# Kernel tuning notes

Hardware: AMD Instinct MI355X
Metric: run time of the kernel (lower is better)

## Reference

```python
import jax, jax.numpy as jnp
import numpy as np

D_MODEL = 512
N_HEADS = 8
HEAD_SIZE = 64


def setup_inputs() -> dict:
    key = jax.random.key(0)
    ks = jax.random.split(key, 6)
    B, T = 4, 2048
    x_q = jax.random.normal(ks[0], (B, T, D_MODEL), dtype=jnp.float32)
    s = 1.0 / np.sqrt(D_MODEL)
    # per-head q/k/v projection weights, stacked: [H, head_size, d_model]
    Wq = jax.random.normal(ks[1], (N_HEADS, HEAD_SIZE, D_MODEL), dtype=jnp.float32) * s
    Wk = jax.random.normal(ks[2], (N_HEADS, HEAD_SIZE, D_MODEL), dtype=jnp.float32) * s
    Wv = jax.random.normal(ks[3], (N_HEADS, HEAD_SIZE, D_MODEL), dtype=jnp.float32) * s
    Wp = jax.random.normal(ks[4], (D_MODEL, D_MODEL), dtype=jnp.float32) * s
    bp = jax.random.normal(ks[5], (D_MODEL,), dtype=jnp.float32) * 0.01
    return {"x_q": x_q, "Wq": Wq, "Wk": Wk, "Wv": Wv, "Wp": Wp, "bp": bp}


def reference(x_q, Wq, Wk, Wv, Wp, bp):
    B, T, C = x_q.shape  # C == d_model
    # per-head projections: [B, H, T, K]
    q = jnp.einsum('btd,hkd->bhtk', x_q, Wq)
    k = jnp.einsum('btd,hkd->bhtk', x_q, Wk)
    v = jnp.einsum('btd,hkd->bhtk', x_q, Wv)
    # NOTE: original scales by C**-0.5 with C = d_model (not head_size)
    scores = jnp.einsum('bhtk,bhsk->bhts', q, k) * (C ** -0.5)
    causal = jnp.tril(jnp.ones((T, T), dtype=bool))
    scores = jnp.where(causal, scores, -jnp.inf)
    wei = jax.nn.softmax(scores, axis=-1)  # dropout is identity in eval
    out = jnp.einsum('bhts,bhsk->bhtk', wei, v)
    # concat heads: [B, T, H*K] == [B, T, d_model]
    out = out.transpose(0, 2, 1, 3).reshape(B, T, C)
    return out @ Wp.T + bp
```

## Files before the change

kernel.cpp:

```cpp
#include <hip/hip_runtime.h>
#include <hip/hip_bf16.h>

using bf16x8 = __attribute__((ext_vector_type(8))) __bf16;
using f32x4  = __attribute__((ext_vector_type(4))) float;
using f32x16 = __attribute__((ext_vector_type(16))) float;
using i32x4  = __attribute__((ext_vector_type(4))) int;

#define MFMA_16x16x32(a, b, c) __builtin_amdgcn_mfma_f32_16x16x32_bf16((a), (b), (c), 0, 0, 0)
#define MFMA32(a, b, c)        __builtin_amdgcn_mfma_f32_32x32x16_bf16((a), (b), (c), 0, 0, 0)

__device__ __forceinline__ ushort f2bf(float f) {
    return __builtin_bit_cast(ushort, (__bf16)f);
}
__device__ __forceinline__ unsigned pk_bf16(float lo, float hi) {
    unsigned r;
    asm volatile("v_cvt_pk_bf16_f32 %0, %1, %2" : "=v"(r) : "v"(lo), "v"(hi));
    return r;
}
__device__ __forceinline__ void pl32_swap(unsigned &a, unsigned &b) {
    asm volatile("v_permlane32_swap_b32 %0, %1" : "+v"(a), "+v"(b));
}

__global__ __launch_bounds__(256) void cvt_bf16(
    const float* __restrict__ in, ushort* __restrict__ out, int n)
{
    const int i = (blockIdx.x * 256 + threadIdx.x) * 8;
    if (i + 8 <= n) {
        const f32x4 a = *(const f32x4*)(in + i);
        const f32x4 b = *(const f32x4*)(in + i + 4);
        union { ushort u[8]; i32x4 w; } p;
        #pragma unroll
        for (int j = 0; j < 4; ++j) { p.u[j] = f2bf(a[j]); p.u[4 + j] = f2bf(b[j]); }
        *(i32x4*)(out + i) = p.w;
    }
}

__global__ __launch_bounds__(256) void gemm_qkv3(
    const ushort* __restrict__ A, const float* __restrict__ Wq,
    const float* __restrict__ Wk, const float* __restrict__ Wv,
    float qscale, ushort* __restrict__ qb, ushort* __restrict__ kb,
    ushort* __restrict__ vb)
{
    __shared__ ushort lA[128][40];
    __shared__ ushort lB[128][40];
    const int wsel = blockIdx.y >> 2;
    const int n0 = (blockIdx.y & 3) * 128;
    const float* W = (wsel == 0) ? Wq : ((wsel == 1) ? Wk : Wv);
    ushort* out = (wsel == 0) ? qb : ((wsel == 1) ? kb : vb);
    const float scale = (wsel == 0) ? qscale : 1.0f;

    const int m0 = blockIdx.x * 128;
    const int tid  = threadIdx.x;
    const int lane = tid & 63;
    const int wave = tid >> 6;
    const int wr = (wave >> 1) * 64, wc = (wave & 1) * 64;
    const int frow = lane & 15, fk = (lane >> 4) * 8;
    const int sr = tid >> 1, scc = (tid & 1) * 16;

    f32x4 acc[4][4] = {};

    for (int k0 = 0; k0 < 512; k0 += 32) {
        const ushort* pa = A + (m0 + sr) * 512 + k0 + scc;
        const i32x4 va0 = *(const i32x4*)(pa);
        const i32x4 va1 = *(const i32x4*)(pa + 8);
        const float* pb = W + (n0 + sr) * 512 + k0 + scc;
        const f32x4 b0 = *(const f32x4*)(pb);
        const f32x4 b1 = *(const f32x4*)(pb + 4);
        const f32x4 b2 = *(const f32x4*)(pb + 8);
        const f32x4 b3 = *(const f32x4*)(pb + 12);
        union { ushort u[16]; i32x4 w[2]; } pB;
        #pragma unroll
        for (int j = 0; j < 4; ++j) {
            pB.u[j]      = f2bf(b0[j]);  pB.u[4 + j]  = f2bf(b1[j]);
            pB.u[8 + j]  = f2bf(b2[j]);  pB.u[12 + j] = f2bf(b3[j]);
        }
        __syncthreads();
        *(i32x4*)&lA[sr][scc]     = va0;
        *(i32x4*)&lA[sr][scc + 8] = va1;
        *(i32x4*)&lB[sr][scc]     = pB.w[0];
        *(i32x4*)&lB[sr][scc + 8] = pB.w[1];
        __syncthreads();

        bf16x8 af[4], bg[4];
        #pragma unroll
        for (int m = 0; m < 4; ++m) af[m] = *(const bf16x8*)&lA[wr + m * 16 + frow][fk];
        #pragma unroll
        for (int n = 0; n < 4; ++n) bg[n] = *(const bf16x8*)&lB[wc + n * 16 + frow][fk];
        #pragma unroll
        for (int m = 0; m < 4; ++m)
            #pragma unroll
            for (int n = 0; n < 4; ++n)
                acc[m][n] = MFMA_16x16x32(af[m], bg[n], acc[m][n]);
    }

    const int rbase = (lane >> 4) * 4;
    const int ccol  = lane & 15;
    if (wsel == 2) {
        #pragma unroll
        for (int m = 0; m < 4; ++m)
            #pragma unroll
            for (int n = 0; n < 4; ++n) {
                const int col = n0 + wc + n * 16 + ccol;
                const int row0 = m0 + wr + m * 16 + rbase;
                unsigned long long u = 0;
                #pragma unroll
                for (int r = 0; r < 4; ++r)
                    u |= ((unsigned long long)f2bf(acc[m][n][r])) << (16 * r);
                const size_t idx = ((size_t)((row0 >> 11) * 8 + (col >> 6)) * 64
                                    + (col & 63)) * 2048 + (row0 & 2047);
                *(unsigned long long*)(out + idx) = u;
            }
    } else {
        #pragma unroll
        for (int m = 0; m < 4; ++m)
            #pragma unroll
            for (int n = 0; n < 4; ++n) {
                const int col = n0 + wc + n * 16 + ccol;
                #pragma unroll
                for (int r = 0; r < 4; ++r) {
                    const int row = m0 + wr + m * 16 + rbase + r;
                    out[(((row >> 11) * 8 + (col >> 6)) * 2048 + (row & 2047)) * 64 + (col & 63)]
                        = f2bf(acc[m][n][r] * scale);
                }
            }
    }
}

__global__ __launch_bounds__(256) void gemm_out(
    const ushort* __restrict__ A, const float* __restrict__ W,
    const float* __restrict__ bias, float* __restrict__ out)
{
    __shared__ ushort lA[128][40];
    __shared__ ushort lB[128][40];
    const int m0 = blockIdx.x * 128;
    const int n0 = blockIdx.y * 128;
    const int tid  = threadIdx.x;
    const int lane = tid & 63;
    const int wave = tid >> 6;
    const int wr = (wave >> 1) * 64, wc = (wave & 1) * 64;
    const int frow = lane & 15, fk = (lane >> 4) * 8;
    const int sr = tid >> 1, scc = (tid & 1) * 16;

    f32x4 acc[4][4] = {};

    for (int k0 = 0; k0 < 512; k0 += 32) {
        const int row = m0 + sr, c = k0 + scc;
        const ushort* pa = A + ((((row >> 11) * 8 + (c >> 6)) * 2048 + (row & 2047)) * 64 + (c & 63));
        const i32x4 va0 = *(const i32x4*)(pa);
        const i32x4 va1 = *(const i32x4*)(pa + 8);
        const float* pb = W + (n0 + sr) * 512 + k0 + scc;
        const f32x4 b0 = *(const f32x4*)(pb);
        const f32x4 b1 = *(const f32x4*)(pb + 4);
        const f32x4 b2 = *(const f32x4*)(pb + 8);
        const f32x4 b3 = *(const f32x4*)(pb + 12);
        union { ushort u[16]; i32x4 w[2]; } pB;
        #pragma unroll
        for (int j = 0; j < 4; ++j) {
            pB.u[j]      = f2bf(b0[j]);  pB.u[4 + j]  = f2bf(b1[j]);
            pB.u[8 + j]  = f2bf(b2[j]);  pB.u[12 + j] = f2bf(b3[j]);
        }
        __syncthreads();
        *(i32x4*)&lA[sr][scc]     = va0;
        *(i32x4*)&lA[sr][scc + 8] = va1;
        *(i32x4*)&lB[sr][scc]     = pB.w[0];
        *(i32x4*)&lB[sr][scc + 8] = pB.w[1];
        __syncthreads();

        bf16x8 af[4], bg[4];
        #pragma unroll
        for (int m = 0; m < 4; ++m) af[m] = *(const bf16x8*)&lA[wr + m * 16 + frow][fk];
        #pragma unroll
        for (int n = 0; n < 4; ++n) bg[n] = *(const bf16x8*)&lB[wc + n * 16 + frow][fk];
        #pragma unroll
        for (int m = 0; m < 4; ++m)
            #pragma unroll
            for (int n = 0; n < 4; ++n)
                acc[m][n] = MFMA_16x16x32(af[m], bg[n], acc[m][n]);
    }

    const int rbase = (lane >> 4) * 4;
    const int ccol  = lane & 15;
    #pragma unroll
    for (int m = 0; m < 4; ++m)
        #pragma unroll
        for (int n = 0; n < 4; ++n) {
            const int col = n0 + wc + n * 16 + ccol;
            const float bv = bias[col];
            #pragma unroll
            for (int r = 0; r < 4; ++r) {
                const int row = m0 + wr + m * 16 + rbase + r;
                out[row * 512 + col] = acc[m][n][r] + bv;
            }
        }
}

__global__ __launch_bounds__(256, 2) void attn_kernel(
    const ushort* __restrict__ q, const ushort* __restrict__ k,
    const ushort* __restrict__ vt, ushort* __restrict__ att)
{
    __shared__ ushort lK[2][64][64];
    __shared__ ushort lV[2][64][64];

    const int NB   = (int)(gridDim.x * gridDim.y);
    const int NH   = NB >> 4;
    const int half = NB >> 1;
    const int n    = (int)(blockIdx.y * gridDim.x + blockIdx.x);
    const int r    = (n < half) ? n : (NB - 1 - (n - half));
    const int qt0  = (15 - r / NH) * 128;
    const int bh   = r % NH;

    const ushort* Q  = q  + (size_t)bh * 2048 * 64;
    const ushort* K  = k  + (size_t)bh * 2048 * 64;
    const ushort* VT = vt + (size_t)bh * 2048 * 64;
    ushort* O = att + (size_t)bh * 2048 * 64;

    const int tid = threadIdx.x;
    const int wv  = tid >> 6;
    const int l   = tid & 63;
    const int ql  = l & 31;
    const int hi  = l >> 5;
    const int wrow0 = qt0 + wv * 32;
    const int qrow  = wrow0 + ql;
    const int wmax  = wrow0 + 31;
    const int qkey  = ql & 7;
    const float LOG2E = 1.44269504088896f;

    const int srow = tid >> 2;
    const int sg   = (tid & 3) * 2;
    const int skey = srow & 7;

    bf16x8 aq[4];
    #pragma unroll
    for (int kk = 0; kk < 4; ++kk)
        aq[kk] = *(const bf16x8*)(Q + (size_t)qrow * 64 + kk * 16 + hi * 8);

    f32x16 o0 = {}, o1 = {};
    float mrun = -30000.0f, lrun = 0.0f;
    const int nt = qt0 / 64 + 2;

    i32x4 kr0, kr1, vr0, vr1;
    auto loadG = [&](int s0) {
        const ushort* kp = K + (size_t)(s0 + srow) * 64 + (tid & 3) * 16;
        kr0 = *(const i32x4*)(kp);
        kr1 = *(const i32x4*)(kp + 8);
        const ushort* vp = VT + (size_t)srow * 2048 + s0 + (tid & 3) * 16;
        vr0 = *(const i32x4*)(vp);
        vr1 = *(const i32x4*)(vp + 8);
    };
    auto writeL = [&](int b) {
        *(i32x4*)&lK[b][srow][((sg    ) ^ skey) * 8] = kr0;
        *(i32x4*)&lK[b][srow][((sg + 1) ^ skey) * 8] = kr1;
        *(i32x4*)&lV[b][srow][((sg    ) ^ skey) * 8] = vr0;
        *(i32x4*)&lV[b][srow][((sg + 1) ^ skey) * 8] = vr1;
    };

    loadG(0);
    writeL(0);
    if (nt > 1) loadG(64);

    for (int t = 0; t < nt; ++t) {
        const int p  = t & 1;
        const int s0 = t * 64;
        __syncthreads();
        if (t + 1 < nt) writeL(p ^ 1);
        if (t + 2 < nt) loadG(s0 + 128);

        if (s0 > wmax) continue;

        f32x16 sa = {}, sb = {};
        #pragma unroll
        for (int kk = 0; kk < 4; ++kk) {
            const bf16x8 kb0 = *(const bf16x8*)&lK[p][ql]     [((2 * kk + hi) ^ qkey) * 8];
            const bf16x8 kb1 = *(const bf16x8*)&lK[p][32 + ql][((2 * kk + hi) ^ qkey) * 8];
            sa = MFMA32(kb0, aq[kk], sa);
            sb = MFMA32(kb1, aq[kk], sb);
        }

        if (s0 + 63 > wrow0) {
            #pragma unroll
            for (int rr = 0; rr < 16; ++rr) {
                const int cr = (rr & 3) + 8 * (rr >> 2) + 4 * hi;
                if (s0 + cr > qrow)      sa[rr] = -30000.0f;
                if (s0 + 32 + cr > qrow) sb[rr] = -30000.0f;
            }
        }

        float pmax = sa[0];
        #pragma unroll
        for (int rr = 1; rr < 16; ++rr) pmax = fmaxf(pmax, sa[rr]);
        #pragma unroll
        for (int rr = 0; rr < 16; ++rr) pmax = fmaxf(pmax, sb[rr]);
        pmax = fmaxf(pmax, __shfl_xor(pmax, 32));

        if (__any(pmax > mrun + 8.0f)) {
            const float mnew  = fmaxf(mrun, pmax);
            const float alpha = exp2f((mrun - mnew) * LOG2E);
            mrun = mnew;
            lrun *= alpha;
            #pragma unroll
            for (int rr = 0; rr < 16; ++rr) {
                const float ar = __shfl(alpha, (rr & 3) + 8 * (rr >> 2) + 4 * hi);
                o0[rr] *= ar; o1[rr] *= ar;
            }
        }

        const float mb = mrun * LOG2E;
        float ps = 0.0f;
        #pragma unroll
        for (int rr = 0; rr < 16; ++rr) {
            sa[rr] = exp2f(fmaf(sa[rr], LOG2E, -mb));
            sb[rr] = exp2f(fmaf(sb[rr], LOG2E, -mb));
            ps += sa[rr] + sb[rr];
        }
        ps += __shfl_xor(ps, 32);
        lrun += ps;

        unsigned paw[4][4];
        #pragma unroll
        for (int ks = 0; ks < 4; ++ks) {
            const int e = 2 * ks, f = 2 * ks + 1;
            const int ra = 4 * (e & 3), rb = 4 * (f & 3);
            unsigned A0, A1, B0, B1;
            if (e >> 2) { A0 = pk_bf16(sb[ra], sb[ra + 1]); A1 = pk_bf16(sb[ra + 2], sb[ra + 3]); }
            else        { A0 = pk_bf16(sa[ra], sa[ra + 1]); A1 = pk_bf16(sa[ra + 2], sa[ra + 3]); }
            if (f >> 2) { B0 = pk_bf16(sb[rb], sb[rb + 1]); B1 = pk_bf16(sb[rb + 2], sb[rb + 3]); }
            else        { B0 = pk_bf16(sa[rb], sa[rb + 1]); B1 = pk_bf16(sa[rb + 2], sa[rb + 3]); }
            pl32_swap(A0, B0);
            pl32_swap(A1, B1);
            paw[ks][0] = A0; paw[ks][1] = A1; paw[ks][2] = B0; paw[ks][3] = B1;
        }

        #pragma unroll
        for (int ks = 0; ks < 4; ++ks) {
            union { unsigned w[4]; bf16x8 v; } u;
            u.w[0] = paw[ks][0]; u.w[1] = paw[ks][1];
            u.w[2] = paw[ks][2]; u.w[3] = paw[ks][3];
            const bf16x8 v0 = *(const bf16x8*)&lV[p][ql]     [((2 * ks + hi) ^ qkey) * 8];
            const bf16x8 v1 = *(const bf16x8*)&lV[p][32 + ql][((2 * ks + hi) ^ qkey) * 8];
            o0 = MFMA32(u.v, v0, o0);
            o1 = MFMA32(u.v, v1, o1);
        }
    }

    const float linv = 1.0f / fmaxf(lrun, 1e-30f);
    #pragma unroll
    for (int rr = 0; rr < 16; ++rr) {
        const int cr = (rr & 3) + 8 * (rr >> 2) + 4 * hi;
        const float li = __shfl(linv, cr);
        const int row = wrow0 + cr;
        O[(size_t)row * 64 + ql]      = f2bf(o0[rr] * li);
        O[(size_t)row * 64 + 32 + ql] = f2bf(o1[rr] * li);
    }
}

extern "C" void kernel_launch(void* const* d_in, const int* in_sizes, int n_in,
                              void* d_out, int out_size, void* d_ws, size_t ws_size,
                              hipStream_t stream) {
    const float* x  = (const float*)d_in[0];
    const float* Wq = (const float*)d_in[1];
    const float* Wk = (const float*)d_in[2];
    const float* Wv = (const float*)d_in[3];
    const float* Wp = (const float*)d_in[4];
    const float* bp = (const float*)d_in[5];
    float* out = (float*)d_out;

    const size_t NEL  = 4u * 8u * 2048u * 64u;
    const size_t NELB = 8u * 2048u * 64u;
    const float qscale = 0.04419417382415922f;

    if (ws_size >= 3u * NEL * sizeof(ushort)) {
        ushort* xbf = (ushort*)d_out;
        ushort* qb  = xbf + NEL;
        ushort* kb  = (ushort*)d_ws;
        ushort* vb  = kb + NEL;
        ushort* ab  = vb + NEL;
        hipLaunchKernelGGL(cvt_bf16, dim3((int)(NEL / (256 * 8))), dim3(256), 0, stream,
                           x, xbf, (int)NEL);
        hipLaunchKernelGGL(gemm_qkv3, dim3(64, 12), dim3(256), 0, stream,
                           xbf, Wq, Wk, Wv, qscale, qb, kb, vb);
        hipLaunchKernelGGL(attn_kernel, dim3(16, 32), dim3(256), 0, stream, qb, kb, vb, ab);
        hipLaunchKernelGGL(gemm_out, dim3(64, 4), dim3(256), 0, stream, ab, Wp, bp, out);
    } else {
        ushort* kb = (ushort*)d_ws;
        ushort* vb = kb + NELB;
        ushort* ab = vb + NELB;
        for (int b = 0; b < 4; ++b) {
            const float* xb = x + (size_t)b * 2048u * 512u;
            float* ob = out + (size_t)b * 2048u * 512u;
            ushort* xbf = (ushort*)ob;
            ushort* qb  = xbf + NELB;
            hipLaunchKernelGGL(cvt_bf16, dim3((int)(NELB / (256 * 8))), dim3(256), 0, stream,
                               xb, xbf, (int)NELB);
            hipLaunchKernelGGL(gemm_qkv3, dim3(16, 12), dim3(256), 0, stream,
                               xbf, Wq, Wk, Wv, qscale, qb, kb, vb);
            hipLaunchKernelGGL(attn_kernel, dim3(16, 8), dim3(256), 0, stream, qb, kb, vb, ab);
            hipLaunchKernelGGL(gemm_out, dim3(16, 4), dim3(256), 0, stream, ab, Wp, bp, ob);
        }
    }
}
```

Measured before the change: 109.9 us.

## Pre-convert QKV weights to bf16 and prefetch next k-tile in GEMMs

Adds a cvt_w3 kernel that converts Wq/Wk/Wv to bf16 once into workspace (reusing the attention output buffer before attention writes it). gemm_qkv3 then loads bf16 weights directly, with no per-tile fp32 loads or conversions that every M-block used to repeat. Both GEMMs also register-prefetch the next k-tile after the LDS store, overlapping global loads with MFMA work. The cost is an extra kernel launch and more live registers.

```diff
diff --git a/kernel.cpp b/kernel.cpp
--- a/kernel.cpp
+++ b/kernel.cpp
@@ -35,9 +35,23 @@
     }
 }
 
+__global__ __launch_bounds__(256) void cvt_w3(
+    const float* __restrict__ w0, const float* __restrict__ w1,
+    const float* __restrict__ w2, ushort* __restrict__ out)
+{
+    const int i = (blockIdx.x * 256 + threadIdx.x) * 8;
+    const int w = i >> 18, off = i & 262143;
+    const float* src = (w == 0) ? w0 : ((w == 1) ? w1 : w2);
+    const f32x4 a = *(const f32x4*)(src + off);
+    const f32x4 b = *(const f32x4*)(src + off + 4);
+    union { ushort u[8]; i32x4 v; } p;
+    #pragma unroll
+    for (int j = 0; j < 4; ++j) { p.u[j] = f2bf(a[j]); p.u[4 + j] = f2bf(b[j]); }
+    *(i32x4*)(out + i) = p.v;
+}
+
 __global__ __launch_bounds__(256) void gemm_qkv3(
-    const ushort* __restrict__ A, const float* __restrict__ Wq,
-    const float* __restrict__ Wk, const float* __restrict__ Wv,
+    const ushort* __restrict__ A, const ushort* __restrict__ Wbf,
     float qscale, ushort* __restrict__ qb, ushort* __restrict__ kb,
     ushort* __restrict__ vb)
 {
@@ -45,7 +59,7 @@
     __shared__ ushort lB[128][40];
     const int wsel = blockIdx.y >> 2;
     const int n0 = (blockIdx.y & 3) * 128;
-    const float* W = (wsel == 0) ? Wq : ((wsel == 1) ? Wk : Wv);
+    const ushort* W = Wbf + wsel * 262144;
     ushort* out = (wsel == 0) ? qb : ((wsel == 1) ? kb : vb);
     const float scale = (wsel == 0) ? qscale : 1.0f;
 
@@ -58,27 +72,24 @@
     const int sr = tid >> 1, scc = (tid & 1) * 16;
 
     f32x4 acc[4][4] = {};
-
-    for (int k0 = 0; k0 < 512; k0 += 32) {
+    i32x4 va0, va1, vb0, vb1;
+    auto load = [&](int k0) {
         const ushort* pa = A + (m0 + sr) * 512 + k0 + scc;
-        const i32x4 va0 = *(const i32x4*)(pa);
-        const i32x4 va1 = *(const i32x4*)(pa + 8);
-        const float* pb = W + (n0 + sr) * 512 + k0 + scc;
-        const f32x4 b0 = *(const f32x4*)(pb);
-        const f32x4 b1 = *(const f32x4*)(pb + 4);
-        const f32x4 b2 = *(const f32x4*)(pb + 8);
-        const f32x4 b3 = *(const f32x4*)(pb + 12);
-        union { ushort u[16]; i32x4 w[2]; } pB;
-        #pragma unroll
-        for (int j = 0; j < 4; ++j) {
-            pB.u[j]      = f2bf(b0[j]);  pB.u[4 + j]  = f2bf(b1[j]);
-            pB.u[8 + j]  = f2bf(b2[j]);  pB.u[12 + j] = f2bf(b3[j]);
-        }
+        va0 = *(const i32x4*)(pa);
+        va1 = *(const i32x4*)(pa + 8);
+        const ushort* pb = W + (n0 + sr) * 512 + k0 + scc;
+        vb0 = *(const i32x4*)(pb);
+        vb1 = *(const i32x4*)(pb + 8);
+    };
+
+    load(0);
+    for (int t = 0; t < 16; ++t) {
         __syncthreads();
         *(i32x4*)&lA[sr][scc]     = va0;
         *(i32x4*)&lA[sr][scc + 8] = va1;
-        *(i32x4*)&lB[sr][scc]     = pB.w[0];
-        *(i32x4*)&lB[sr][scc + 8] = pB.w[1];
+        *(i32x4*)&lB[sr][scc]     = vb0;
+        *(i32x4*)&lB[sr][scc + 8] = vb1;
+        if (t + 1 < 16) load((t + 1) * 32);
         __syncthreads();
 
         bf16x8 af[4], bg[4];
@@ -142,17 +153,22 @@
     const int sr = tid >> 1, scc = (tid & 1) * 16;
 
     f32x4 acc[4][4] = {};
-
-    for (int k0 = 0; k0 < 512; k0 += 32) {
+    i32x4 va0, va1;
+    f32x4 b0, b1, b2, b3;
+    auto load = [&](int k0) {
         const int row = m0 + sr, c = k0 + scc;
         const ushort* pa = A + ((((row >> 11) * 8 + (c >> 6)) * 2048 + (row & 2047)) * 64 + (c & 63));
-        const i32x4 va0 = *(const i32x4*)(pa);
-        const i32x4 va1 = *(const i32x4*)(pa + 8);
+        va0 = *(const i32x4*)(pa);
+        va1 = *(const i32x4*)(pa + 8);
         const float* pb = W + (n0 + sr) * 512 + k0 + scc;
-        const f32x4 b0 = *(const f32x4*)(pb);
-        const f32x4 b1 = *(const f32x4*)(pb + 4);
-        const f32x4 b2 = *(const f32x4*)(pb + 8);
-        const f32x4 b3 = *(const f32x4*)(pb + 12);
+        b0 = *(const f32x4*)(pb);
+        b1 = *(const f32x4*)(pb + 4);
+        b2 = *(const f32x4*)(pb + 8);
+        b3 = *(const f32x4*)(pb + 12);
+    };
+
+    load(0);
+    for (int t = 0; t < 16; ++t) {
         union { ushort u[16]; i32x4 w[2]; } pB;
         #pragma unroll
         for (int j = 0; j < 4; ++j) {
@@ -164,6 +180,7 @@
         *(i32x4*)&lA[sr][scc + 8] = va1;
         *(i32x4*)&lB[sr][scc]     = pB.w[0];
         *(i32x4*)&lB[sr][scc + 8] = pB.w[1];
+        if (t + 1 < 16) load((t + 1) * 32);
         __syncthreads();
 
         bf16x8 af[4], bg[4];
@@ -374,16 +391,19 @@
         ushort* kb  = (ushort*)d_ws;
         ushort* vb  = kb + NEL;
         ushort* ab  = vb + NEL;
+        ushort* wbf = ab;
         hipLaunchKernelGGL(cvt_bf16, dim3((int)(NEL / (256 * 8))), dim3(256), 0, stream,
                            x, xbf, (int)NEL);
+        hipLaunchKernelGGL(cvt_w3, dim3(384), dim3(256), 0, stream, Wq, Wk, Wv, wbf);
         hipLaunchKernelGGL(gemm_qkv3, dim3(64, 12), dim3(256), 0, stream,
-                           xbf, Wq, Wk, Wv, qscale, qb, kb, vb);
+                           xbf, wbf, qscale, qb, kb, vb);
         hipLaunchKernelGGL(attn_kernel, dim3(16, 32), dim3(256), 0, stream, qb, kb, vb, ab);
         hipLaunchKernelGGL(gemm_out, dim3(64, 4), dim3(256), 0, stream, ab, Wp, bp, out);
     } else {
         ushort* kb = (ushort*)d_ws;
         ushort* vb = kb + NELB;
         ushort* ab = vb + NELB;
+        ushort* wbf = ab;
         for (int b = 0; b < 4; ++b) {
             const float* xb = x + (size_t)b * 2048u * 512u;
             float* ob = out + (size_t)b * 2048u * 512u;
@@ -391,8 +411,9 @@
             ushort* qb  = xbf + NELB;
             hipLaunchKernelGGL(cvt_bf16, dim3((int)(NELB / (256 * 8))), dim3(256), 0, stream,
                                xb, xbf, (int)NELB);
+            hipLaunchKernelGGL(cvt_w3, dim3(384), dim3(256), 0, stream, Wq, Wk, Wv, wbf);
             hipLaunchKernelGGL(gemm_qkv3, dim3(16, 12), dim3(256), 0, stream,
-                               xbf, Wq, Wk, Wv, qscale, qb, kb, vb);
+                               xbf, wbf, qscale, qb, kb, vb);
             hipLaunchKernelGGL(attn_kernel, dim3(16, 8), dim3(256), 0, stream, qb, kb, vb, ab);
             hipLaunchKernelGGL(gemm_out, dim3(16, 4), dim3(256), 0, stream, ab, Wp, bp, ob);
         }
```

New measurement: 106.5 us. 1.03x faster.
